# Optimization experiments

Hardware: AMD Instinct MI355X
Metric: run time of the kernel (lower is better)

## Reference

```python
import jax, jax.numpy as jnp
import numpy as np

BN_EPS = 1e-5


def _batchnorm(x, gamma, beta):
    # BatchNorm1d in training mode: per-batch mean and biased variance
    mean = jnp.mean(x, axis=0)
    var = jnp.mean((x - mean) ** 2, axis=0)
    return gamma * (x - mean) / jnp.sqrt(var + BN_EPS) + beta


def setup_inputs() -> dict:
    key = jax.random.key(0)
    ks = jax.random.split(key, 8)
    N, D, H, C = 400000, 192, 192, 8
    inputs = jax.random.normal(ks[0], (N, D), dtype=jnp.float32)
    labels = jax.random.randint(ks[1], (N,), 0, C, dtype=jnp.int64)
    s = 0.05
    return {
        "inputs": inputs,
        "labels": labels,
        "W1": jax.random.normal(ks[2], (D, H), dtype=jnp.float32) * s,
        "b1": jnp.zeros((H,), dtype=jnp.float32),
        "g1": jnp.ones((H,), dtype=jnp.float32),
        "be1": jnp.zeros((H,), dtype=jnp.float32),
        "W2": jax.random.normal(ks[3], (H, H), dtype=jnp.float32) * s,
        "b2": jnp.zeros((H,), dtype=jnp.float32),
        "g2": jnp.ones((H,), dtype=jnp.float32),
        "be2": jnp.zeros((H,), dtype=jnp.float32),
        "W3": jax.random.normal(ks[4], (H, C), dtype=jnp.float32) * s,
        "b3": jnp.zeros((C,), dtype=jnp.float32),
    }


def reference(inputs, labels, W1, b1, g1, be1, W2, b2, g2, be2, W3, b3):
    # The per-unique-label mask/concat loop is equivalent to a stable sort by label
    order = jnp.argsort(labels, stable=True)
    fea = inputs[order]              # [N, D]
    domain_ids = labels[order]       # [N]
    # ReverseLayerF is identity in the forward pass
    h = jax.nn.relu(_batchnorm(fea @ W1 + b1, g1, be1))
    h = jax.nn.relu(_batchnorm(h @ W2 + b2, g2, be2))
    pred = jax.nn.sigmoid(h @ W3 + b3)   # [N, C]
    logp = jax.nn.log_softmax(pred, axis=-1)
    loss = -jnp.mean(jnp.take_along_axis(logp, domain_ids[:, None], axis=1))
    return loss
```

## Files before the change

### kernel.cpp

```cpp
#include <hip/hip_runtime.h>

typedef unsigned char u8;
typedef unsigned int u32;
typedef long long i64;
typedef __attribute__((ext_vector_type(2))) float f32x2;
typedef __attribute__((ext_vector_type(4))) float f32x4;

#define NROWS 400000
#define DIM 192
#define GRPB 64
#define GNBLK (NROWS / GRPB)
#define FRPB 128
#define FNBLK (NROWS / FRPB)
#define SLAB 25
#define RBLK (GNBLK / SLAB)
#define PITCH 200
#define BN_EPS 1e-5f

#if __has_builtin(__builtin_amdgcn_cvt_pk_fp8_f32) && __has_builtin(__builtin_amdgcn_cvt_pk_f32_fp8)
#define HW_FP8 1
#endif

__device__ __forceinline__ u32 enc1_fp8(float f) {
  float a = fabsf(f);
  u32 sg = (__float_as_uint(f) >> 24) & 0x80u;
  a = fminf(a, 448.f);
  u32 em;
  if (a >= 0.015625f) {
    u32 b = __float_as_uint(a);
    b += 0x0007FFFFu + ((b >> 20) & 1u);
    em = ((b >> 20) & 0xFFFu) - 960u;
  } else {
    em = (u32)(int)rintf(a * 512.f);
  }
  return sg | em;
}

__device__ __forceinline__ u32 pack4_fp8(float f0, float f1, float f2, float f3) {
#ifdef HW_FP8
  int w = 0;
  w = __builtin_amdgcn_cvt_pk_fp8_f32(f0, f1, w, false);
  w = __builtin_amdgcn_cvt_pk_fp8_f32(f2, f3, w, true);
  return (u32)w;
#else
  return enc1_fp8(f0) | (enc1_fp8(f1) << 8) | (enc1_fp8(f2) << 16) | (enc1_fp8(f3) << 24);
#endif
}

#ifndef HW_FP8
__device__ __forceinline__ float dec1_fp8(u32 b) {
  u32 em = b & 0x7Fu;
  float vn = __uint_as_float((em + 960u) << 20);
  float vd = (float)em * 0.001953125f;
  float v = (em >= 8u) ? vn : vd;
  return (b & 0x80u) ? -v : v;
}
#endif

__device__ __forceinline__ void unpack8_fp8(uint2 p, float (&f)[8]) {
#ifdef HW_FP8
  f32x2 v0 = __builtin_amdgcn_cvt_pk_f32_fp8(p.x, false);
  f32x2 v1 = __builtin_amdgcn_cvt_pk_f32_fp8(p.x, true);
  f32x2 v2 = __builtin_amdgcn_cvt_pk_f32_fp8(p.y, false);
  f32x2 v3 = __builtin_amdgcn_cvt_pk_f32_fp8(p.y, true);
  f[0] = v0[0]; f[1] = v0[1]; f[2] = v1[0]; f[3] = v1[1];
  f[4] = v2[0]; f[5] = v2[1]; f[6] = v3[0]; f[7] = v3[1];
#else
#pragma unroll
  for (int i = 0; i < 4; ++i) f[i] = dec1_fp8((p.x >> (8 * i)) & 0xFFu);
#pragma unroll
  for (int i = 0; i < 4; ++i) f[4 + i] = dec1_fp8((p.y >> (8 * i)) & 0xFFu);
#endif
}

__device__ __forceinline__ i64 u2l(uint2 u) {
  union { uint2 u2; i64 l; } c; c.u2 = u; return c.l;
}

__global__ void prep_w(const float* __restrict__ W1, const float* __restrict__ W2,
                       const float* __restrict__ W3, u8* __restrict__ W1q,
                       u8* __restrict__ W2q, u8* __restrict__ W3q) {
  int idx = blockIdx.x * 256 + threadIdx.x;
  if (idx < DIM * DIM) {
    int h = idx / DIM, d = idx % DIM;
    W1q[idx] = (u8)enc1_fp8(W1[d * DIM + h]);
    W2q[idx] = (u8)enc1_fp8(W2[d * DIM + h]);
  } else if (idx < DIM * DIM + 16 * DIM) {
    int j = idx - DIM * DIM;
    int c = j / DIM, k = j % DIM;
    W3q[j] = (c < 8) ? (u8)enc1_fp8(W3[k * 8 + c]) : (u8)0;
  }
}

template <int LAYER>
__global__ __launch_bounds__(256, LAYER == 1 ? 3 : 4) void gemm_bn(
    const float* __restrict__ Xf, const u8* __restrict__ Yin8,
    u8* __restrict__ Yout8, const u8* __restrict__ Wq,
    const float* __restrict__ scale_in, const float* __restrict__ shift_in,
    float* __restrict__ partials) {
  __shared__ __align__(16) char smem[GRPB * PITCH];
  const int t = threadIdx.x;
  const int bid = blockIdx.x;
  const size_t row0 = (size_t)bid * GRPB;

  const int lane = t & 63, wv = t >> 6;
  const int cb = wv * 48;
  const int lr = lane & 15;
  const int g = lane >> 4;
  const int kg = g * 8;

  i64 wf0[6], wf1[6], wf2[6];
#pragma unroll
  for (int ks = 0; ks < 6; ++ks) {
    const int k0 = ks * 32 + kg;
    wf0[ks] = u2l(*(const uint2*)(Wq + (size_t)(cb + lr) * DIM + k0));
    wf1[ks] = u2l(*(const uint2*)(Wq + (size_t)(cb + 16 + lr) * DIM + k0));
    wf2[ks] = u2l(*(const uint2*)(Wq + (size_t)(cb + 32 + lr) * DIM + k0));
  }

  if (LAYER == 1) {
    const float4* Xv = (const float4*)(Xf + row0 * DIM);
#pragma unroll
    for (int j = 0; j < 12; ++j) {
      int e = j * 256 + t;
      int r = e / 48, c4 = e % 48;
      float4 v = Xv[e];
      *(u32*)(smem + r * PITCH + c4 * 4) = pack4_fp8(v.x, v.y, v.z, v.w);
    }
  } else {
    const uint2* Yin2 = (const uint2*)(Yin8 + row0 * DIM);
#pragma unroll
    for (int j = 0; j < 6; ++j) {
      int e = j * 256 + t;
      int r = e / 24, c8 = e % 24;
      int cb8 = c8 * 8;
      uint2 p = Yin2[r * 24 + c8];
      float f[8];
      unpack8_fp8(p, f);
      float4 sc0 = *(const float4*)&scale_in[cb8];
      float4 sc1 = *(const float4*)&scale_in[cb8 + 4];
      float4 sh0 = *(const float4*)&shift_in[cb8];
      float4 sh1 = *(const float4*)&shift_in[cb8 + 4];
      float scv[8] = {sc0.x, sc0.y, sc0.z, sc0.w, sc1.x, sc1.y, sc1.z, sc1.w};
      float shv[8] = {sh0.x, sh0.y, sh0.z, sh0.w, sh1.x, sh1.y, sh1.z, sh1.w};
      float h[8];
#pragma unroll
      for (int i = 0; i < 8; ++i) h[i] = fmaxf(f[i] * scv[i] + shv[i], 0.f);
      uint2 o;
      o.x = pack4_fp8(h[0], h[1], h[2], h[3]);
      o.y = pack4_fp8(h[4], h[5], h[6], h[7]);
      *(uint2*)(smem + r * PITCH + cb8) = o;
    }
  }
  __syncthreads();

  f32x4 acc[4][3];
#pragma unroll
  for (int rt = 0; rt < 4; ++rt)
#pragma unroll
    for (int ct = 0; ct < 3; ++ct) acc[rt][ct] = (f32x4){0.f, 0.f, 0.f, 0.f};

#pragma unroll
  for (int ks = 0; ks < 6; ++ks) {
    const int k0 = ks * 32 + kg;
#pragma unroll
    for (int rt = 0; rt < 4; ++rt) {
      i64 a = u2l(*(const uint2*)(smem + (rt * 16 + lr) * PITCH + k0));
      acc[rt][0] = __builtin_amdgcn_mfma_f32_16x16x32_fp8_fp8(wf0[ks], a, acc[rt][0], 0, 0, 0);
      acc[rt][1] = __builtin_amdgcn_mfma_f32_16x16x32_fp8_fp8(wf1[ks], a, acc[rt][1], 0, 0, 0);
      acc[rt][2] = __builtin_amdgcn_mfma_f32_16x16x32_fp8_fp8(wf2[ks], a, acc[rt][2], 0, 0, 0);
    }
  }
  __syncthreads();

  f32x4 s[3], q[3];
#pragma unroll
  for (int ct = 0; ct < 3; ++ct) { s[ct] = (f32x4){0,0,0,0}; q[ct] = (f32x4){0,0,0,0}; }
  u32* lds32 = (u32*)smem;
#pragma unroll
  for (int rt = 0; rt < 4; ++rt) {
    const int row = rt * 16 + lr;
#pragma unroll
    for (int ct = 0; ct < 3; ++ct) {
      f32x4 v = acc[rt][ct];
      s[ct][0] += v[0]; s[ct][1] += v[1]; s[ct][2] += v[2]; s[ct][3] += v[3];
      q[ct][0] += v[0]*v[0]; q[ct][1] += v[1]*v[1]; q[ct][2] += v[2]*v[2]; q[ct][3] += v[3]*v[3];
      lds32[row * 50 + wv * 12 + ct * 4 + g] = pack4_fp8(v[0], v[1], v[2], v[3]);
    }
  }
  __syncthreads();

  uint4* Yo4 = (uint4*)(Yout8 + row0 * DIM);
#pragma unroll
  for (int u = 0; u < 3; ++u) {
    int idx4 = u * 256 + t;
    int row = idx4 / 12, m = idx4 % 12;
    uint2 a = *(const uint2*)&lds32[row * 50 + m * 4];
    uint2 b = *(const uint2*)&lds32[row * 50 + m * 4 + 2];
    Yo4[idx4] = (uint4){a.x, a.y, b.x, b.y};
  }

#pragma unroll
  for (int ct = 0; ct < 3; ++ct)
#pragma unroll
    for (int off = 1; off <= 8; off <<= 1)
#pragma unroll
      for (int i = 0; i < 4; ++i) {
        s[ct][i] += __shfl_xor(s[ct][i], off);
        q[ct][i] += __shfl_xor(q[ct][i], off);
      }
  if (lr == 0) {
    size_t base = (size_t)bid * 384 + cb + g * 4;
#pragma unroll
    for (int ct = 0; ct < 3; ++ct) {
      *(f32x4*)&partials[base + ct * 16] = s[ct];
      *(f32x4*)&partials[base + ct * 16 + 192] = q[ct];
    }
  }
}

__global__ __launch_bounds__(384) void bn_reduce1(const float* __restrict__ partials,
                                                  float* __restrict__ out2) {
  const int b = blockIdx.x, t = threadIdx.x;
  const float* p = partials + (size_t)b * SLAB * 384;
  float v = 0.f;
#pragma unroll
  for (int r = 0; r < SLAB; ++r) v += p[r * 384 + t];
  out2[b * 384 + t] = v;
}

__global__ __launch_bounds__(384) void bn_fin2(
    const float* __restrict__ out2, const float* __restrict__ g,
    const float* __restrict__ be, float* __restrict__ scale,
    float* __restrict__ shift, float* accum) {
  __shared__ float tot[384];
  const int t = threadIdx.x;
  float v = 0.f;
  for (int b = 0; b < RBLK; ++b) v += out2[b * 384 + t];
  tot[t] = v;
  __syncthreads();
  if (t < 192) {
    float s = tot[t], q = tot[t + 192];
    float mean = s / (float)NROWS;
    float var = q / (float)NROWS - mean * mean;
    float inv = rsqrtf(var + BN_EPS);
    float sc = g[t] * inv;
    scale[t] = sc;
    shift[t] = be[t] - mean * sc;
  }
  if (t == 0) *accum = 0.f;
}

__global__ __launch_bounds__(256, 4) void final_loss(
    const u8* __restrict__ Y2, const int* __restrict__ labels,
    const float* __restrict__ scale2, const float* __restrict__ shift2,
    const u8* __restrict__ W3q, const float* __restrict__ b3, float* accum) {
  __shared__ __align__(16) char smem[FRPB * PITCH];
  __shared__ __align__(16) float sc2[DIM], sh2[DIM];
  __shared__ float red[4];
  const int t = threadIdx.x;
  const size_t row0 = (size_t)blockIdx.x * FRPB;
  const int lane = t & 63, wv = t >> 6;
  const int lr = lane & 15, g = lane >> 4, kg = g * 8;

  i64 wf[6];
#pragma unroll
  for (int ks = 0; ks < 6; ++ks)
    wf[ks] = u2l(*(const uint2*)(W3q + lr * DIM + ks * 32 + kg));
  const float b3v = (lr < 8) ? b3[lr] : 0.f;

  if (t < 48) ((float4*)sc2)[t] = ((const float4*)scale2)[t];
  else if (t < 96) ((float4*)sh2)[t - 48] = ((const float4*)shift2)[t - 48];
  __syncthreads();

  const uint4* Yp4 = (const uint4*)(Y2 + row0 * DIM);
#pragma unroll
  for (int j = 0; j < 6; ++j) {
    int idx4 = j * 256 + t;
    int row = idx4 / 12, c0 = (idx4 % 12) * 16;
    uint4 p = Yp4[idx4];
    uint2 plo = {p.x, p.y}, phi = {p.z, p.w};
    float fa[8], fb[8];
    unpack8_fp8(plo, fa);
    unpack8_fp8(phi, fb);
    float h[16];
#pragma unroll
    for (int i = 0; i < 8; ++i) {
      h[i] = fmaxf(fa[i] * sc2[c0 + i] + sh2[c0 + i], 0.f);
      h[8 + i] = fmaxf(fb[i] * sc2[c0 + 8 + i] + sh2[c0 + 8 + i], 0.f);
    }
    uint2 o0 = {pack4_fp8(h[0], h[1], h[2], h[3]), pack4_fp8(h[4], h[5], h[6], h[7])};
    uint2 o1 = {pack4_fp8(h[8], h[9], h[10], h[11]), pack4_fp8(h[12], h[13], h[14], h[15])};
    *(uint2*)(smem + row * PITCH + c0) = o0;
    *(uint2*)(smem + row * PITCH + c0 + 8) = o1;
  }
  __syncthreads();

  float contrib = 0.f;
#pragma unroll
  for (int tl = 0; tl < 2; ++tl) {
    const int rbase = wv * 32 + tl * 16;
    f32x4 acc = (f32x4){0.f, 0.f, 0.f, 0.f};
#pragma unroll
    for (int ks = 0; ks < 6; ++ks) {
      const int k0 = ks * 32 + kg;
      i64 a = u2l(*(const uint2*)(smem + (rbase + lr) * PITCH + k0));
      acc = __builtin_amdgcn_mfma_f32_16x16x32_fp8_fp8(a, wf[ks], acc, 0, 0, 0);
    }
#pragma unroll
    for (int i = 0; i < 4; ++i) {
      float pv = 1.f / (1.f + __expf(-(acc[i] + b3v)));
      float m = pv;
      m = fmaxf(m, __shfl_xor(m, 1));
      m = fmaxf(m, __shfl_xor(m, 2));
      m = fmaxf(m, __shfl_xor(m, 4));
      float e = __expf(pv - m);
      e += __shfl_xor(e, 1);
      e += __shfl_xor(e, 2);
      e += __shfl_xor(e, 4);
      int lab = labels[row0 + rbase + g * 4 + i];
      if (lr == lab) contrib += m + __logf(e) - pv;
    }
  }
#pragma unroll
  for (int off = 1; off < 64; off <<= 1) contrib += __shfl_xor(contrib, off);
  if (lane == 0) red[wv] = contrib;
  __syncthreads();
  if (t == 0) atomicAdd(accum, red[0] + red[1] + red[2] + red[3]);
}

__global__ void finalize(const float* __restrict__ accum, float* __restrict__ out) {
  if (threadIdx.x == 0) out[0] = accum[0] / (float)NROWS;
}

extern "C" void kernel_launch(void* const* d_in, const int* in_sizes, int n_in,
                              void* d_out, int out_size, void* d_ws, size_t ws_size,
                              hipStream_t stream) {
  const float* inputs = (const float*)d_in[0];
  const int* labels   = (const int*)d_in[1];
  const float* W1  = (const float*)d_in[2];
  const float* g1  = (const float*)d_in[4];
  const float* be1 = (const float*)d_in[5];
  const float* W2  = (const float*)d_in[6];
  const float* g2  = (const float*)d_in[8];
  const float* be2 = (const float*)d_in[9];
  const float* W3  = (const float*)d_in[10];
  const float* b3  = (const float*)d_in[11];
  float* out = (float*)d_out;

  char* ws = (char*)d_ws;
  u8* W1q       = (u8*)(ws + 0);
  u8* W2q       = (u8*)(ws + 40960);
  u8* W3q       = (u8*)(ws + 81920);
  float* scale1 = (float*)(ws + 98304);
  float* shift1 = (float*)(ws + 99072);
  float* scale2 = (float*)(ws + 99840);
  float* shift2 = (float*)(ws + 100608);
  float* accum  = (float*)(ws + 101376);
  float* out2   = (float*)(ws + 102400);
  float* partials = (float*)(ws + 524288);
  u8* Ybuf      = (u8*)(ws + 16777216);

  prep_w<<<156, 256, 0, stream>>>(W1, W2, W3, W1q, W2q, W3q);
  gemm_bn<1><<<GNBLK, 256, 0, stream>>>(inputs, nullptr, Ybuf, W1q, nullptr, nullptr, partials);
  bn_reduce1<<<RBLK, 384, 0, stream>>>(partials, out2);
  bn_fin2<<<1, 384, 0, stream>>>(out2, g1, be1, scale1, shift1, accum);
  gemm_bn<2><<<GNBLK, 256, 0, stream>>>(nullptr, Ybuf, Ybuf, W2q, scale1, shift1, partials);
  bn_reduce1<<<RBLK, 384, 0, stream>>>(partials, out2);
  bn_fin2<<<1, 384, 0, stream>>>(out2, g2, be2, scale2, shift2, accum);
  final_loss<<<FNBLK, 256, 0, stream>>>(Ybuf, labels, scale2, shift2, W3q, b3, accum);
  finalize<<<1, 64, 0, stream>>>(accum, out);
}
```

Before: 224.1 us.

## Replace BN partial-sum reduction kernels with bucketed atomics and last-block finalize

Each GEMM block now atomically adds its per-column sum and sum-of-squares into one of 64 bucketed stat arrays instead of writing a per-block partial row, so the separate bn_reduce1 pass disappears and bn_fin sums only 64 buckets. The loss kernel uses a completion counter so the last block writes the final mean, removing the finalize launch. Zeroing of the stat buckets, accumulator and counter moves into prep_w. This cuts two to three kernel launches and a pass over the partials buffer, at the cost of global atomic contention (384 atomics per block) and non-deterministic float summation order.

```diff
diff --git a/kernel.cpp b/kernel.cpp
--- a/kernel.cpp
+++ b/kernel.cpp
@@ -12,8 +12,7 @@
 #define GNBLK (NROWS / GRPB)
 #define FRPB 128
 #define FNBLK (NROWS / FRPB)
-#define SLAB 25
-#define RBLK (GNBLK / SLAB)
+#define NBUCKET 64
 #define PITCH 200
 #define BN_EPS 1e-5f
 
@@ -79,8 +78,12 @@
 
 __global__ void prep_w(const float* __restrict__ W1, const float* __restrict__ W2,
                        const float* __restrict__ W3, u8* __restrict__ W1q,
-                       u8* __restrict__ W2q, u8* __restrict__ W3q) {
+                       u8* __restrict__ W2q, u8* __restrict__ W3q,
+                       float* __restrict__ stats1, float* __restrict__ stats2,
+                       float* __restrict__ accum, u32* __restrict__ counter) {
   int idx = blockIdx.x * 256 + threadIdx.x;
+  if (idx < NBUCKET * 384) { stats1[idx] = 0.f; stats2[idx] = 0.f; }
+  if (idx == 0) { *accum = 0.f; *counter = 0u; }
   if (idx < DIM * DIM) {
     int h = idx / DIM, d = idx % DIM;
     W1q[idx] = (u8)enc1_fp8(W1[d * DIM + h]);
@@ -97,7 +100,7 @@
     const float* __restrict__ Xf, const u8* __restrict__ Yin8,
     u8* __restrict__ Yout8, const u8* __restrict__ Wq,
     const float* __restrict__ scale_in, const float* __restrict__ shift_in,
-    float* __restrict__ partials) {
+    float* __restrict__ stats) {
   __shared__ __align__(16) char smem[GRPB * PITCH];
   const int t = threadIdx.x;
   const int bid = blockIdx.x;
@@ -210,33 +213,27 @@
         q[ct][i] += __shfl_xor(q[ct][i], off);
       }
   if (lr == 0) {
-    size_t base = (size_t)bid * 384 + cb + g * 4;
-#pragma unroll
-    for (int ct = 0; ct < 3; ++ct) {
-      *(f32x4*)&partials[base + ct * 16] = s[ct];
-      *(f32x4*)&partials[base + ct * 16 + 192] = q[ct];
-    }
-  }
-}
-
-__global__ __launch_bounds__(384) void bn_reduce1(const float* __restrict__ partials,
-                                                  float* __restrict__ out2) {
-  const int b = blockIdx.x, t = threadIdx.x;
-  const float* p = partials + (size_t)b * SLAB * 384;
-  float v = 0.f;
-#pragma unroll
-  for (int r = 0; r < SLAB; ++r) v += p[r * 384 + t];
-  out2[b * 384 + t] = v;
-}
-
-__global__ __launch_bounds__(384) void bn_fin2(
-    const float* __restrict__ out2, const float* __restrict__ g,
+    float* bucket = stats + (size_t)(bid & (NBUCKET - 1)) * 384;
+#pragma unroll
+    for (int ct = 0; ct < 3; ++ct)
+#pragma unroll
+      for (int i = 0; i < 4; ++i) {
+        int c = cb + ct * 16 + g * 4 + i;
+        atomicAdd(&bucket[c], s[ct][i]);
+        atomicAdd(&bucket[c + 192], q[ct][i]);
+      }
+  }
+}
+
+__global__ __launch_bounds__(384) void bn_fin(
+    const float* __restrict__ stats, const float* __restrict__ g,
     const float* __restrict__ be, float* __restrict__ scale,
-    float* __restrict__ shift, float* accum) {
+    float* __restrict__ shift) {
   __shared__ float tot[384];
   const int t = threadIdx.x;
   float v = 0.f;
-  for (int b = 0; b < RBLK; ++b) v += out2[b * 384 + t];
+#pragma unroll
+  for (int b = 0; b < NBUCKET; ++b) v += stats[b * 384 + t];
   tot[t] = v;
   __syncthreads();
   if (t < 192) {
@@ -248,13 +245,14 @@
     scale[t] = sc;
     shift[t] = be[t] - mean * sc;
   }
-  if (t == 0) *accum = 0.f;
 }
 
 __global__ __launch_bounds__(256, 4) void final_loss(
     const u8* __restrict__ Y2, const int* __restrict__ labels,
     const float* __restrict__ scale2, const float* __restrict__ shift2,
-    const u8* __restrict__ W3q, const float* __restrict__ b3, float* accum) {
+    const u8* __restrict__ W3q, const float* __restrict__ b3,
+    float* __restrict__ accum, u32* __restrict__ counter,
+    float* __restrict__ out) {
   __shared__ __align__(16) char smem[FRPB * PITCH];
   __shared__ __align__(16) float sc2[DIM], sh2[DIM];
   __shared__ float red[4];
@@ -326,11 +324,15 @@
   for (int off = 1; off < 64; off <<= 1) contrib += __shfl_xor(contrib, off);
   if (lane == 0) red[wv] = contrib;
   __syncthreads();
-  if (t == 0) atomicAdd(accum, red[0] + red[1] + red[2] + red[3]);
-}
-
-__global__ void finalize(const float* __restrict__ accum, float* __restrict__ out) {
-  if (threadIdx.x == 0) out[0] = accum[0] / (float)NROWS;
+  if (t == 0) {
+    atomicAdd(accum, red[0] + red[1] + red[2] + red[3]);
+    __threadfence();
+    u32 prev = atomicAdd(counter, 1u);
+    if (prev == (u32)(FNBLK - 1)) {
+      float a = *(volatile float*)accum;
+      out[0] = a / (float)NROWS;
+    }
+  }
 }
 
 extern "C" void kernel_launch(void* const* d_in, const int* in_sizes, int n_in,
@@ -357,17 +359,15 @@
   float* scale2 = (float*)(ws + 99840);
   float* shift2 = (float*)(ws + 100608);
   float* accum  = (float*)(ws + 101376);
-  float* out2   = (float*)(ws + 102400);
-  float* partials = (float*)(ws + 524288);
+  u32* counter  = (u32*)(ws + 101440);
+  float* stats1 = (float*)(ws + 131072);
+  float* stats2 = (float*)(ws + 262144);
   u8* Ybuf      = (u8*)(ws + 16777216);
 
-  prep_w<<<156, 256, 0, stream>>>(W1, W2, W3, W1q, W2q, W3q);
-  gemm_bn<1><<<GNBLK, 256, 0, stream>>>(inputs, nullptr, Ybuf, W1q, nullptr, nullptr, partials);
-  bn_reduce1<<<RBLK, 384, 0, stream>>>(partials, out2);
-  bn_fin2<<<1, 384, 0, stream>>>(out2, g1, be1, scale1, shift1, accum);
-  gemm_bn<2><<<GNBLK, 256, 0, stream>>>(nullptr, Ybuf, Ybuf, W2q, scale1, shift1, partials);
-  bn_reduce1<<<RBLK, 384, 0, stream>>>(partials, out2);
-  bn_fin2<<<1, 384, 0, stream>>>(out2, g2, be2, scale2, shift2, accum);
-  final_loss<<<FNBLK, 256, 0, stream>>>(Ybuf, labels, scale2, shift2, W3q, b3, accum);
-  finalize<<<1, 64, 0, stream>>>(accum, out);
-}
+  prep_w<<<156, 256, 0, stream>>>(W1, W2, W3, W1q, W2q, W3q, stats1, stats2, accum, counter);
+  gemm_bn<1><<<GNBLK, 256, 0, stream>>>(inputs, nullptr, Ybuf, W1q, nullptr, nullptr, stats1);
+  bn_fin<<<1, 384, 0, stream>>>(stats1, g1, be1, scale1, shift1);
+  gemm_bn<2><<<GNBLK, 256, 0, stream>>>(nullptr, Ybuf, Ybuf, W2q, scale1, shift1, stats2);
+  bn_fin<<<1, 384, 0, stream>>>(stats2, g2, be2, scale2, shift2);
+  final_loss<<<FNBLK, 256, 0, stream>>>(Ybuf, labels, scale2, shift2, W3q, b3, accum, counter, out);
+}
```

New measurement: 257.8 us (median of 2 runs). +15.0%, slower.
